# Kernel optimization log

Hardware: AMD Instinct MI355X
Metric: run time of the kernel (lower is better)

## Reference

```python
import jax, jax.numpy as jnp
import numpy as np
import math

N, E = 50000, 600000
IN_DIM, H, C, EDGE_DIM, OUT_DIM, PE_DIM = 128, 4, 32, 32, 64, 16
HC = H * C  # concat output dim of each TransformerConv layer


def _leaky(t):
    # nn.LeakyReLU default negative_slope = 0.01
    return jnp.where(t > 0, t, 0.01 * t)


def _conv(x, src, dst, edge_attr, Wq, bq, Wk, bk, Wv, bv, We, Wsk, bsk):
    """PyG TransformerConv (beta=False, concat=True, root_weight=True)."""
    n = x.shape[0]
    q = (x @ Wq + bq).reshape(n, H, C)
    k = (x @ Wk + bk).reshape(n, H, C)
    v = (x @ Wv + bv).reshape(n, H, C)
    e = (edge_attr @ We).reshape(-1, H, C)  # lin_edge has no bias
    k_j = k[src] + e                         # [E,H,C]
    alpha = jnp.einsum('ehc,ehc->eh', q[dst], k_j) / math.sqrt(C)  # [E,H]
    # segment softmax over incoming edges of each destination node
    m = jax.ops.segment_max(alpha, dst, num_segments=n)
    a = jnp.exp(alpha - m[dst])
    denom = jax.ops.segment_sum(a, dst, num_segments=n)
    a = a / denom[dst]
    v_j = v[src] + e                         # [E,H,C]
    out = jax.ops.segment_sum(a[..., None] * v_j, dst, num_segments=n)
    return out.reshape(n, HC) + x @ Wsk + bsk  # skip (root) connection


def setup_inputs() -> dict:
    key = jax.random.key(0)
    keys = iter(jax.random.split(key, 40))

    def nrm(shape, scale=1.0):
        return jax.random.normal(next(keys), shape, jnp.float32) * scale

    inp = {
        'x': nrm((N, IN_DIM)),
        'pe': nrm((N, PE_DIM)),
        'edge_index': jax.random.randint(next(keys), (2, E), 0, N),
        'edge_attr': nrm((E, EDGE_DIM)),
        'batch': jnp.zeros((N,), jnp.int32),
    }
    fins = [IN_DIM, HC]
    for l in range(2):
        fin = fins[l]
        s = 1.0 / math.sqrt(fin)
        se = 1.0 / math.sqrt(EDGE_DIM)
        for nm in ['Wq', 'Wk', 'Wv', 'Wsk']:
            inp[f'{nm}{l}'] = nrm((fin, HC), s)
        inp[f'We{l}'] = nrm((EDGE_DIM, HC), se)
        for nm in ['bq', 'bk', 'bv', 'bsk']:
            inp[f'{nm}{l}'] = jnp.zeros((HC,), jnp.float32)
    inp['W1'] = nrm((HC, C), 1.0 / math.sqrt(HC))
    inp['b1'] = jnp.zeros((C,), jnp.float32)
    inp['W2'] = nrm((C, OUT_DIM), 1.0 / math.sqrt(C))
    inp['b2'] = jnp.zeros((OUT_DIM,), jnp.float32)
    return inp


def reference(x, pe, edge_index, edge_attr, batch,
              Wq0, bq0, Wk0, bk0, Wv0, bv0, We0, Wsk0, bsk0,
              Wq1, bq1, Wk1, bk1, Wv1, bv1, We1, Wsk1, bsk1,
              W1, b1, W2, b2):
    src, dst = edge_index[0], edge_index[1]
    h = _leaky(_conv(x, src, dst, edge_attr, Wq0, bq0, Wk0, bk0, Wv0, bv0, We0, Wsk0, bsk0))
    h = _leaky(_conv(h, src, dst, edge_attr, Wq1, bq1, Wk1, bk1, Wv1, bv1, We1, Wsk1, bsk1))
    return _leaky(h @ W1 + b1) @ W2 + b2
```

## Files before the change

### kernel.cpp

```cpp
#include <hip/hip_runtime.h>
#include <hip/hip_bf16.h>
#include <math.h>

#define NN 50000
#define NE 600000

__global__ __launch_bounds__(256) void hist_kernel(const int* __restrict__ dst,
                                                   int* __restrict__ deg, int E) {
    int e = blockIdx.x * 256 + threadIdx.x;
    if (e < E) atomicAdd(&deg[dst[e]], 1);
}

__global__ __launch_bounds__(256) void scan_kernel(const int* __restrict__ deg,
                                                   int* __restrict__ indptr,
                                                   int* __restrict__ cursor, int n) {
    __shared__ int wsum[4];
    __shared__ int carry_s;
    const int tid = threadIdx.x, lane = tid & 63, wv = tid >> 6;
    if (tid == 0) carry_s = 0;
    __syncthreads();
    const int nceil = (n + 1023) & ~1023;
    for (int base = 0; base < nceil; base += 1024) {
        int i = base + tid * 4;
        int4 v = make_int4(0, 0, 0, 0);
        if (i + 3 < n) v = *(const int4*)(deg + i);
        else {
            if (i < n)     v.x = deg[i];
            if (i + 1 < n) v.y = deg[i + 1];
            if (i + 2 < n) v.z = deg[i + 2];
            if (i + 3 < n) v.w = deg[i + 3];
        }
        int tsum = v.x + v.y + v.z + v.w;
        int incl = tsum;
        #pragma unroll
        for (int off = 1; off < 64; off <<= 1) {
            int u = __shfl_up(incl, off);
            if (lane >= off) incl += u;
        }
        if (lane == 63) wsum[wv] = incl;
        __syncthreads();
        int wpre = 0;
        for (int w = 0; w < wv; ++w) wpre += wsum[w];
        int carry = carry_s;
        int start = carry + wpre + incl - tsum;
        if (i < n)     { indptr[i] = start;           cursor[i] = start; }
        int s1 = start + v.x;
        if (i + 1 < n) { indptr[i + 1] = s1;          cursor[i + 1] = s1; }
        int s2 = s1 + v.y;
        if (i + 2 < n) { indptr[i + 2] = s2;          cursor[i + 2] = s2; }
        int s3 = s2 + v.z;
        if (i + 3 < n) { indptr[i + 3] = s3;          cursor[i + 3] = s3; }
        __syncthreads();
        if (tid == 255) carry_s = carry + wpre + incl;
        __syncthreads();
    }
    if (tid == 0) indptr[n] = carry_s;
}

__global__ __launch_bounds__(256) void scatter_kernel(const int* __restrict__ src,
                                                      const int* __restrict__ dst,
                                                      int* __restrict__ cursor,
                                                      int* __restrict__ src_csr,
                                                      int* __restrict__ eid_csr, int E) {
    int e = blockIdx.x * 256 + threadIdx.x;
    if (e < E) {
        int d = dst[e];
        int slot = atomicAdd(&cursor[d], 1);
        src_csr[slot] = src[e];
        eid_csr[slot] = e;
    }
}

__global__ __launch_bounds__(256) void permute_ea(const int* __restrict__ eid_csr,
                                                  const float* __restrict__ ea,
                                                  float* __restrict__ ea_csr, int E) {
    int g = blockIdx.x * 256 + threadIdx.x;
    if (g < E * 8) {
        int slot = g >> 3, q = g & 7;
        int eid = eid_csr[slot];
        ((float4*)ea_csr)[(size_t)slot * 8 + q] = ((const float4*)ea)[(size_t)eid * 8 + q];
    }
}

__global__ __launch_bounds__(256, 4) void qkvsk_gemm(const float* __restrict__ X,
        const float* __restrict__ Wq,  const float* __restrict__ bq,
        const float* __restrict__ Wk,  const float* __restrict__ bk,
        const float* __restrict__ Wv,  const float* __restrict__ bv,
        const float* __restrict__ Wsk, const float* __restrict__ bsk,
        float* __restrict__ out, int nrows) {
    __shared__ float XsT[32][68];
    __shared__ float Ws[32][132];
    const int mat = blockIdx.y;
    const float* __restrict__ W;
    const float* __restrict__ bias;
    switch (mat) {
        case 0:  W = Wq;  bias = bq;  break;
        case 1:  W = Wk;  bias = bk;  break;
        case 2:  W = Wv;  bias = bv;  break;
        default: W = Wsk; bias = bsk; break;
    }
    const int n0 = blockIdx.x * 64;
    const int tid = threadIdx.x;
    const int tc = tid & 15;
    const int tr = tid >> 4;
    float acc[4][8];
    #pragma unroll
    for (int i = 0; i < 4; ++i)
        #pragma unroll
        for (int j = 0; j < 8; ++j) acc[i][j] = 0.f;

    #pragma unroll 1
    for (int k0 = 0; k0 < 128; k0 += 32) {
        #pragma unroll
        for (int c = 0; c < 2; ++c) {
            int lin4 = tid + c * 256;
            int row = lin4 >> 3, kq = lin4 & 7;
            int gr = n0 + row;
            float4 v = make_float4(0.f, 0.f, 0.f, 0.f);
            if (gr < nrows) v = ((const float4*)X)[(size_t)gr * 32 + (k0 >> 2) + kq];
            XsT[kq * 4 + 0][row] = v.x;
            XsT[kq * 4 + 1][row] = v.y;
            XsT[kq * 4 + 2][row] = v.z;
            XsT[kq * 4 + 3][row] = v.w;
        }
        #pragma unroll
        for (int c = 0; c < 4; ++c) {
            int lin4 = tid + c * 256;
            int row = lin4 >> 5, c4 = lin4 & 31;
            float4 v = ((const float4*)W)[(size_t)(k0 + row) * 32 + c4];
            Ws[row][c4 * 4 + 0] = v.x; Ws[row][c4 * 4 + 1] = v.y;
            Ws[row][c4 * 4 + 2] = v.z; Ws[row][c4 * 4 + 3] = v.w;
        }
        __syncthreads();
        #pragma unroll 8
        for (int k = 0; k < 32; ++k) {
            float4 xv = *(const float4*)&XsT[k][tr * 4];
            float4 w0 = *(const float4*)&Ws[k][tc * 8];
            float4 w1 = *(const float4*)&Ws[k][tc * 8 + 4];
            float xf[4] = {xv.x, xv.y, xv.z, xv.w};
            #pragma unroll
            for (int i = 0; i < 4; ++i) {
                acc[i][0] += xf[i] * w0.x; acc[i][1] += xf[i] * w0.y;
                acc[i][2] += xf[i] * w0.z; acc[i][3] += xf[i] * w0.w;
                acc[i][4] += xf[i] * w1.x; acc[i][5] += xf[i] * w1.y;
                acc[i][6] += xf[i] * w1.z; acc[i][7] += xf[i] * w1.w;
            }
        }
        __syncthreads();
    }
    float bfrag[8];
    #pragma unroll
    for (int j = 0; j < 8; ++j) bfrag[j] = bias[tc * 8 + j];
    #pragma unroll
    for (int i = 0; i < 4; ++i) {
        int gr = n0 + tr * 4 + i;
        if (gr < nrows) {
            float* orow = out + (size_t)gr * 512 + mat * 128 + tc * 8;
            float4 o0 = make_float4(acc[i][0] + bfrag[0], acc[i][1] + bfrag[1],
                                    acc[i][2] + bfrag[2], acc[i][3] + bfrag[3]);
            float4 o1 = make_float4(acc[i][4] + bfrag[4], acc[i][5] + bfrag[5],
                                    acc[i][6] + bfrag[6], acc[i][7] + bfrag[7]);
            *(float4*)orow = o0;
            *(float4*)(orow + 4) = o1;
        }
    }
}

template <bool PERM>
__global__ __launch_bounds__(256) void attn_kernel(const float* __restrict__ qkvsk,
                                                   const int* __restrict__ indptr,
                                                   const int* __restrict__ src_csr,
                                                   const int* __restrict__ eid_csr,
                                                   const float* __restrict__ ea,
                                                   const float* __restrict__ We,
                                                   float* __restrict__ hout, int nnodes) {
    __shared__ float We_s[32 * 128];
    for (int i = threadIdx.x; i < 1024; i += 256)
        ((float4*)We_s)[i] = ((const float4*)We)[i];
    __syncthreads();

    const int lane = threadIdx.x & 63;
    const int n = blockIdx.x * 4 + (threadIdx.x >> 6);
    if (n >= nnodes) return;

    const int d0 = lane * 2;
    const int h = lane >> 4;
    const int i0 = (lane & 15) * 2;

    const float2* nrow = (const float2*)(qkvsk + (size_t)n * 512);
    const float2 q2 = nrow[lane];

    float t0 = 0.f, t1 = 0.f;
    {
        const float4* qh = (const float4*)(qkvsk + (size_t)n * 512 + h * 32);
        #pragma unroll
        for (int c4 = 0; c4 < 8; ++c4) {
            float4 qv = qh[c4];
            int cb = h * 32 + c4 * 4;
            float4 w0 = *(const float4*)&We_s[i0 * 128 + cb];
            float4 w1 = *(const float4*)&We_s[(i0 + 1) * 128 + cb];
            t0 += qv.x * w0.x + qv.y * w0.y + qv.z * w0.z + qv.w * w0.w;
            t1 += qv.x * w1.x + qv.y * w1.y + qv.z * w1.z + qv.w * w1.w;
        }
    }

    float m = -INFINITY, ssum = 0.f;
    float accvx = 0.f, accvy = 0.f, accex = 0.f, accey = 0.f;
    const int s_end = indptr[n + 1];
    for (int s = indptr[n]; s < s_end; ++s) {
        int src = src_csr[s];
        size_t erow = PERM ? (size_t)s * 32 : (size_t)eid_csr[s] * 32;
        float2 ea2 = *(const float2*)(ea + erow + i0);
        const float2* srow = (const float2*)(qkvsk + (size_t)src * 512);
        float2 k2 = srow[64 + lane];
        float p = q2.x * k2.x + q2.y * k2.y + ea2.x * t0 + ea2.y * t1;
        p += __shfl_xor(p, 1);
        p += __shfl_xor(p, 2);
        p += __shfl_xor(p, 4);
        p += __shfl_xor(p, 8);
        float alpha = p * 0.17677669529663687f;
        float mnew = fmaxf(m, alpha);
        float sc = __expf(m - mnew);
        float a = __expf(alpha - mnew);
        m = mnew;
        ssum = ssum * sc + a;
        float2 v2 = srow[128 + lane];
        accvx = accvx * sc + a * v2.x;
        accvy = accvy * sc + a * v2.y;
        accex = accex * sc + a * ea2.x;
        accey = accey * sc + a * ea2.y;
    }

    float e0 = 0.f, e1 = 0.f;
    const int gbase = lane & 48;
    #pragma unroll
    for (int ii = 0; ii < 16; ++ii) {
        float ax = __shfl(accex, gbase + ii);
        float ay = __shfl(accey, gbase + ii);
        int ia = ii * 2;
        float2 wA = *(const float2*)&We_s[ia * 128 + d0];
        float2 wB = *(const float2*)&We_s[(ia + 1) * 128 + d0];
        e0 += ax * wA.x + ay * wB.x;
        e1 += ax * wA.y + ay * wB.y;
    }

    float inv = (ssum > 0.f) ? 1.0f / ssum : 0.f;
    float2 sk2 = nrow[192 + lane];
    float o0 = (accvx + e0) * inv + sk2.x;
    float o1 = (accvy + e1) * inv + sk2.y;
    o0 = o0 > 0.f ? o0 : 0.01f * o0;
    o1 = o1 > 0.f ? o1 : 0.01f * o1;
    ((float2*)(hout + (size_t)n * 128))[lane] = make_float2(o0, o1);
}

__global__ __launch_bounds__(256) void mlp_kernel(const float* __restrict__ h,
                                                  const float* __restrict__ W1,
                                                  const float* __restrict__ b1,
                                                  const float* __restrict__ W2,
                                                  const float* __restrict__ b2,
                                                  float* __restrict__ out, int nnodes) {
    __shared__ float W1s[128 * 32];
    __shared__ float W2s[32 * 64];
    __shared__ float b1s[32], b2s[64];
    for (int i = threadIdx.x; i < 1024; i += 256)
        ((float4*)W1s)[i] = ((const float4*)W1)[i];
    for (int i = threadIdx.x; i < 512; i += 256)
        ((float4*)W2s)[i] = ((const float4*)W2)[i];
    if (threadIdx.x < 32) b1s[threadIdx.x] = b1[threadIdx.x];
    if (threadIdx.x < 64) b2s[threadIdx.x] = b2[threadIdx.x];
    __syncthreads();

    const int j = threadIdx.x & 31;
    const int n = blockIdx.x * 8 + (threadIdx.x >> 5);
    if (n >= nnodes) return;

    const float4* h4 = (const float4*)(h + (size_t)n * 128);
    float t = b1s[j];
    #pragma unroll
    for (int k4 = 0; k4 < 32; ++k4) {
        float4 hv = h4[k4];
        t += hv.x * W1s[(k4 * 4 + 0) * 32 + j];
        t += hv.y * W1s[(k4 * 4 + 1) * 32 + j];
        t += hv.z * W1s[(k4 * 4 + 2) * 32 + j];
        t += hv.w * W1s[(k4 * 4 + 3) * 32 + j];
    }
    t = t > 0.f ? t : 0.01f * t;

    float o0 = b2s[j], o1 = b2s[j + 32];
    const int base = threadIdx.x & 32;
    #pragma unroll
    for (int c = 0; c < 32; ++c) {
        float tc = __shfl(t, base + c);
        o0 += tc * W2s[c * 64 + j];
        o1 += tc * W2s[c * 64 + j + 32];
    }
    out[(size_t)n * 64 + j] = o0;
    out[(size_t)n * 64 + j + 32] = o1;
}

extern "C" void kernel_launch(void* const* d_in, const int* in_sizes, int n_in,
                              void* d_out, int out_size, void* d_ws, size_t ws_size,
                              hipStream_t stream) {
    const float* x         = (const float*)d_in[0];
    const int*   edge_index= (const int*)d_in[2];
    const float* edge_attr = (const float*)d_in[3];
    const float* Wq0 = (const float*)d_in[5],  *Wk0 = (const float*)d_in[6];
    const float* Wv0 = (const float*)d_in[7],  *Wsk0= (const float*)d_in[8];
    const float* We0 = (const float*)d_in[9];
    const float* bq0 = (const float*)d_in[10], *bk0 = (const float*)d_in[11];
    const float* bv0 = (const float*)d_in[12], *bsk0= (const float*)d_in[13];
    const float* Wq1 = (const float*)d_in[14], *Wk1 = (const float*)d_in[15];
    const float* Wv1 = (const float*)d_in[16], *Wsk1= (const float*)d_in[17];
    const float* We1 = (const float*)d_in[18];
    const float* bq1 = (const float*)d_in[19], *bk1 = (const float*)d_in[20];
    const float* bv1 = (const float*)d_in[21], *bsk1= (const float*)d_in[22];
    const float* W1  = (const float*)d_in[23], *b1  = (const float*)d_in[24];
    const float* W2  = (const float*)d_in[25], *b2  = (const float*)d_in[26];

    const int N = in_sizes[0] / 128;
    const int E = in_sizes[2] / 2;
    const int* src = edge_index;
    const int* dst = edge_index + E;

    char* p = (char*)d_ws;
    size_t used = 0;
    auto alloc = [&](size_t bytes) {
        void* r = p + used;
        used += (bytes + 255) & ~(size_t)255;
        return r;
    };
    int*   indptr  = (int*)alloc((size_t)(N + 1) * 4);
    int*   deg     = (int*)alloc((size_t)N * 4);
    int*   cursor  = (int*)alloc((size_t)N * 4);
    int*   src_csr = (int*)alloc((size_t)E * 4);
    int*   eid_csr = (int*)alloc((size_t)E * 4);
    float* qkvsk   = (float*)alloc((size_t)N * 512 * 4);
    float* h0      = (float*)alloc((size_t)N * 128 * 4);
    float* h1      = (float*)alloc((size_t)N * 128 * 4);
    float* ea_csr  = (float*)alloc((size_t)E * 32 * 4);
    const bool perm_ok = (used <= ws_size);

    (void)hipMemsetAsync(deg, 0, (size_t)N * 4, stream);
    hist_kernel<<<(E + 255) / 256, 256, 0, stream>>>(dst, deg, E);
    scan_kernel<<<1, 256, 0, stream>>>(deg, indptr, cursor, N);
    scatter_kernel<<<(E + 255) / 256, 256, 0, stream>>>(src, dst, cursor, src_csr, eid_csr, E);
    if (perm_ok)
        permute_ea<<<((size_t)E * 8 + 255) / 256, 256, 0, stream>>>(eid_csr, edge_attr, ea_csr, E);

    dim3 ggrid((N + 63) / 64, 4);
    dim3 agrid((N + 3) / 4);

    qkvsk_gemm<<<ggrid, 256, 0, stream>>>(x, Wq0, bq0, Wk0, bk0, Wv0, bv0, Wsk0, bsk0, qkvsk, N);
    if (perm_ok)
        attn_kernel<true><<<agrid, 256, 0, stream>>>(qkvsk, indptr, src_csr, eid_csr, ea_csr, We0, h0, N);
    else
        attn_kernel<false><<<agrid, 256, 0, stream>>>(qkvsk, indptr, src_csr, eid_csr, edge_attr, We0, h0, N);

    qkvsk_gemm<<<ggrid, 256, 0, stream>>>(h0, Wq1, bq1, Wk1, bk1, Wv1, bv1, Wsk1, bsk1, qkvsk, N);
    if (perm_ok)
        attn_kernel<true><<<agrid, 256, 0, stream>>>(qkvsk, indptr, src_csr, eid_csr, ea_csr, We1, h1, N);
    else
        attn_kernel<false><<<agrid, 256, 0, stream>>>(qkvsk, indptr, src_csr, eid_csr, edge_attr, We1, h1, N);

    mlp_kernel<<<(N + 7) / 8, 256, 0, stream>>>(h1, W1, b1, W2, b2, (float*)d_out, N);
}
```

Measured before the change: 951.7 us.

## Split Q/skip and K/V buffers and process two edges per attention iteration

The projection output is split into two contiguous arrays, one holding Q and skip and one holding K and V. Each gathered source row in the attention loop then touches a single compact 1 KB span instead of two regions of a 2 KB row. The attention loop handles two edges per iteration with independent online-softmax states that are merged at the end, so more gathers are in flight at once. The shared-memory We tile is padded to a stride of 132 to reduce bank conflicts. The cost is extra registers for the second accumulator set, which may lower occupancy.

```diff
diff --git a/kernel.cpp b/kernel.cpp
--- a/kernel.cpp
+++ b/kernel.cpp
@@ -1,9 +1,6 @@
 #include <hip/hip_runtime.h>
 #include <hip/hip_bf16.h>
 #include <math.h>
-
-#define NN 50000
-#define NE 600000
 
 __global__ __launch_bounds__(256) void hist_kernel(const int* __restrict__ dst,
                                                    int* __restrict__ deg, int E) {
@@ -87,17 +84,19 @@
         const float* __restrict__ Wk,  const float* __restrict__ bk,
         const float* __restrict__ Wv,  const float* __restrict__ bv,
         const float* __restrict__ Wsk, const float* __restrict__ bsk,
-        float* __restrict__ out, int nrows) {
+        float* __restrict__ qsk, float* __restrict__ kv, int nrows) {
     __shared__ float XsT[32][68];
     __shared__ float Ws[32][132];
     const int mat = blockIdx.y;
     const float* __restrict__ W;
     const float* __restrict__ bias;
+    float* __restrict__ out;
+    int col;
     switch (mat) {
-        case 0:  W = Wq;  bias = bq;  break;
-        case 1:  W = Wk;  bias = bk;  break;
-        case 2:  W = Wv;  bias = bv;  break;
-        default: W = Wsk; bias = bsk; break;
+        case 0:  W = Wq;  bias = bq;  out = qsk; col = 0;   break;
+        case 1:  W = Wk;  bias = bk;  out = kv;  col = 0;   break;
+        case 2:  W = Wv;  bias = bv;  out = kv;  col = 128; break;
+        default: W = Wsk; bias = bsk; out = qsk; col = 128; break;
     }
     const int n0 = blockIdx.x * 64;
     const int tid = threadIdx.x;
@@ -155,7 +154,7 @@
     for (int i = 0; i < 4; ++i) {
         int gr = n0 + tr * 4 + i;
         if (gr < nrows) {
-            float* orow = out + (size_t)gr * 512 + mat * 128 + tc * 8;
+            float* orow = out + (size_t)gr * 256 + col + tc * 8;
             float4 o0 = make_float4(acc[i][0] + bfrag[0], acc[i][1] + bfrag[1],
                                     acc[i][2] + bfrag[2], acc[i][3] + bfrag[3]);
             float4 o1 = make_float4(acc[i][4] + bfrag[4], acc[i][5] + bfrag[5],
@@ -167,16 +166,20 @@
 }
 
 template <bool PERM>
-__global__ __launch_bounds__(256) void attn_kernel(const float* __restrict__ qkvsk,
+__global__ __launch_bounds__(256) void attn_kernel(const float* __restrict__ qsk,
+                                                   const float* __restrict__ kv,
                                                    const int* __restrict__ indptr,
                                                    const int* __restrict__ src_csr,
                                                    const int* __restrict__ eid_csr,
                                                    const float* __restrict__ ea,
                                                    const float* __restrict__ We,
                                                    float* __restrict__ hout, int nnodes) {
-    __shared__ float We_s[32 * 128];
-    for (int i = threadIdx.x; i < 1024; i += 256)
-        ((float4*)We_s)[i] = ((const float4*)We)[i];
+    __shared__ float We_s[32 * 132];
+    for (int i4 = threadIdx.x; i4 < 1024; i4 += 256) {
+        int r = i4 >> 5, c4 = i4 & 31;
+        float4 v = ((const float4*)We)[i4];
+        *((float4*)(We_s + r * 132 + c4 * 4)) = v;
+    }
     __syncthreads();
 
     const int lane = threadIdx.x & 63;
@@ -187,49 +190,106 @@
     const int h = lane >> 4;
     const int i0 = (lane & 15) * 2;
 
-    const float2* nrow = (const float2*)(qkvsk + (size_t)n * 512);
+    const float2* nrow = (const float2*)(qsk + (size_t)n * 256);
     const float2 q2 = nrow[lane];
 
     float t0 = 0.f, t1 = 0.f;
     {
-        const float4* qh = (const float4*)(qkvsk + (size_t)n * 512 + h * 32);
+        const float4* qh = (const float4*)(qsk + (size_t)n * 256 + h * 32);
         #pragma unroll
         for (int c4 = 0; c4 < 8; ++c4) {
             float4 qv = qh[c4];
             int cb = h * 32 + c4 * 4;
-            float4 w0 = *(const float4*)&We_s[i0 * 128 + cb];
-            float4 w1 = *(const float4*)&We_s[(i0 + 1) * 128 + cb];
+            float4 w0 = *(const float4*)&We_s[i0 * 132 + cb];
+            float4 w1 = *(const float4*)&We_s[(i0 + 1) * 132 + cb];
             t0 += qv.x * w0.x + qv.y * w0.y + qv.z * w0.z + qv.w * w0.w;
             t1 += qv.x * w1.x + qv.y * w1.y + qv.z * w1.z + qv.w * w1.w;
         }
     }
 
-    float m = -INFINITY, ssum = 0.f;
-    float accvx = 0.f, accvy = 0.f, accex = 0.f, accey = 0.f;
+    const float scale = 0.17677669529663687f;
+    float mA = -INFINITY, ssA = 0.f, avxA = 0.f, avyA = 0.f, aexA = 0.f, aeyA = 0.f;
+    float mB = -INFINITY, ssB = 0.f, avxB = 0.f, avyB = 0.f, aexB = 0.f, aeyB = 0.f;
+
+    int s = indptr[n];
     const int s_end = indptr[n + 1];
-    for (int s = indptr[n]; s < s_end; ++s) {
-        int src = src_csr[s];
-        size_t erow = PERM ? (size_t)s * 32 : (size_t)eid_csr[s] * 32;
-        float2 ea2 = *(const float2*)(ea + erow + i0);
-        const float2* srow = (const float2*)(qkvsk + (size_t)src * 512);
-        float2 k2 = srow[64 + lane];
-        float p = q2.x * k2.x + q2.y * k2.y + ea2.x * t0 + ea2.y * t1;
-        p += __shfl_xor(p, 1);
-        p += __shfl_xor(p, 2);
-        p += __shfl_xor(p, 4);
-        p += __shfl_xor(p, 8);
-        float alpha = p * 0.17677669529663687f;
-        float mnew = fmaxf(m, alpha);
-        float sc = __expf(m - mnew);
-        float a = __expf(alpha - mnew);
-        m = mnew;
-        ssum = ssum * sc + a;
-        float2 v2 = srow[128 + lane];
-        accvx = accvx * sc + a * v2.x;
-        accvy = accvy * sc + a * v2.y;
-        accex = accex * sc + a * ea2.x;
-        accey = accey * sc + a * ea2.y;
-    }
+    #pragma unroll 1
+    for (; s + 1 < s_end; s += 2) {
+        int srcA = src_csr[s];
+        int srcB = src_csr[s + 1];
+        size_t erowA = PERM ? (size_t)s * 32       : (size_t)eid_csr[s] * 32;
+        size_t erowB = PERM ? (size_t)(s + 1) * 32 : (size_t)eid_csr[s + 1] * 32;
+        float2 eaA = *(const float2*)(ea + erowA + i0);
+        float2 eaB = *(const float2*)(ea + erowB + i0);
+        const float2* rowA = (const float2*)(kv + (size_t)srcA * 256);
+        const float2* rowB = (const float2*)(kv + (size_t)srcB * 256);
+        float2 kA = rowA[lane];
+        float2 kB = rowB[lane];
+        float2 vA = rowA[64 + lane];
+        float2 vB = rowB[64 + lane];
+        float pA = q2.x * kA.x + q2.y * kA.y + eaA.x * t0 + eaA.y * t1;
+        float pB = q2.x * kB.x + q2.y * kB.y + eaB.x * t0 + eaB.y * t1;
+        pA += __shfl_xor(pA, 1);  pB += __shfl_xor(pB, 1);
+        pA += __shfl_xor(pA, 2);  pB += __shfl_xor(pB, 2);
+        pA += __shfl_xor(pA, 4);  pB += __shfl_xor(pB, 4);
+        pA += __shfl_xor(pA, 8);  pB += __shfl_xor(pB, 8);
+        float alA = pA * scale;
+        float alB = pB * scale;
+        {
+            float mn = fmaxf(mA, alA);
+            float sc = __expf(mA - mn);
+            float a  = __expf(alA - mn);
+            mA = mn;
+            ssA  = ssA  * sc + a;
+            avxA = avxA * sc + a * vA.x;
+            avyA = avyA * sc + a * vA.y;
+            aexA = aexA * sc + a * eaA.x;
+            aeyA = aeyA * sc + a * eaA.y;
+        }
+        {
+            float mn = fmaxf(mB, alB);
+            float sc = __expf(mB - mn);
+            float a  = __expf(alB - mn);
+            mB = mn;
+            ssB  = ssB  * sc + a;
+            avxB = avxB * sc + a * vB.x;
+            avyB = avyB * sc + a * vB.y;
+            aexB = aexB * sc + a * eaB.x;
+            aeyB = aeyB * sc + a * eaB.y;
+        }
+    }
+    if (s < s_end) {
+        int srcA = src_csr[s];
+        size_t erowA = PERM ? (size_t)s * 32 : (size_t)eid_csr[s] * 32;
+        float2 eaA = *(const float2*)(ea + erowA + i0);
+        const float2* rowA = (const float2*)(kv + (size_t)srcA * 256);
+        float2 kA = rowA[lane];
+        float2 vA = rowA[64 + lane];
+        float pA = q2.x * kA.x + q2.y * kA.y + eaA.x * t0 + eaA.y * t1;
+        pA += __shfl_xor(pA, 1);
+        pA += __shfl_xor(pA, 2);
+        pA += __shfl_xor(pA, 4);
+        pA += __shfl_xor(pA, 8);
+        float alA = pA * scale;
+        float mn = fmaxf(mA, alA);
+        float sc = __expf(mA - mn);
+        float a  = __expf(alA - mn);
+        mA = mn;
+        ssA  = ssA  * sc + a;
+        avxA = avxA * sc + a * vA.x;
+        avyA = avyA * sc + a * vA.y;
+        aexA = aexA * sc + a * eaA.x;
+        aeyA = aeyA * sc + a * eaA.y;
+    }
+
+    const float mm = fmaxf(mA, mB);
+    const float scA = (mA > -INFINITY) ? __expf(mA - mm) : 0.f;
+    const float scB = (mB > -INFINITY) ? __expf(mB - mm) : 0.f;
+    const float ssum  = ssA * scA + ssB * scB;
+    const float accvx = avxA * scA + avxB * scB;
+    const float accvy = avyA * scA + avyB * scB;
+    const float accex = aexA * scA + aexB * scB;
+    const float accey = aeyA * scA + aeyB * scB;
 
     float e0 = 0.f, e1 = 0.f;
     const int gbase = lane & 48;
@@ -238,14 +298,14 @@
         float ax = __shfl(accex, gbase + ii);
         float ay = __shfl(accey, gbase + ii);
         int ia = ii * 2;
-        float2 wA = *(const float2*)&We_s[ia * 128 + d0];
-        float2 wB = *(const float2*)&We_s[(ia + 1) * 128 + d0];
+        float2 wA = *(const float2*)&We_s[ia * 132 + d0];
+        float2 wB = *(const float2*)&We_s[(ia + 1) * 132 + d0];
         e0 += ax * wA.x + ay * wB.x;
         e1 += ax * wA.y + ay * wB.y;
     }
 
     float inv = (ssum > 0.f) ? 1.0f / ssum : 0.f;
-    float2 sk2 = nrow[192 + lane];
+    float2 sk2 = nrow[64 + lane];
     float o0 = (accvx + e0) * inv + sk2.x;
     float o1 = (accvy + e1) * inv + sk2.y;
     o0 = o0 > 0.f ? o0 : 0.01f * o0;
@@ -334,7 +394,8 @@
     int*   cursor  = (int*)alloc((size_t)N * 4);
     int*   src_csr = (int*)alloc((size_t)E * 4);
     int*   eid_csr = (int*)alloc((size_t)E * 4);
-    float* qkvsk   = (float*)alloc((size_t)N * 512 * 4);
+    float* qsk     = (float*)alloc((size_t)N * 256 * 4);
+    float* kvt     = (float*)alloc((size_t)N * 256 * 4);
     float* h0      = (float*)alloc((size_t)N * 128 * 4);
     float* h1      = (float*)alloc((size_t)N * 128 * 4);
     float* ea_csr  = (float*)alloc((size_t)E * 32 * 4);
@@ -350,17 +411,17 @@
     dim3 ggrid((N + 63) / 64, 4);
     dim3 agrid((N + 3) / 4);
 
-    qkvsk_gemm<<<ggrid, 256, 0, stream>>>(x, Wq0, bq0, Wk0, bk0, Wv0, bv0, Wsk0, bsk0, qkvsk, N);
+    qkvsk_gemm<<<ggrid, 256, 0, stream>>>(x, Wq0, bq0, Wk0, bk0, Wv0, bv0, Wsk0, bsk0, qsk, kvt, N);
     if (perm_ok)
-        attn_kernel<true><<<agrid, 256, 0, stream>>>(qkvsk, indptr, src_csr, eid_csr, ea_csr, We0, h0, N);
+        attn_kernel<true><<<agrid, 256, 0, stream>>>(qsk, kvt, indptr, src_csr, eid_csr, ea_csr, We0, h0, N);
     else
-        attn_kernel<false><<<agrid, 256, 0, stream>>>(qkvsk, indptr, src_csr, eid_csr, edge_attr, We0, h0, N);
-
-    qkvsk_gemm<<<ggrid, 256, 0, stream>>>(h0, Wq1, bq1, Wk1, bk1, Wv1, bv1, Wsk1, bsk1, qkvsk, N);
+        attn_kernel<false><<<agrid, 256, 0, stream>>>(qsk, kvt, indptr, src_csr, eid_csr, edge_attr, We0, h0, N);
+
+    qkvsk_gemm<<<ggrid, 256, 0, stream>>>(h0, Wq1, bq1, Wk1, bk1, Wv1, bv1, Wsk1, bsk1, qsk, kvt, N);
     if (perm_ok)
-        attn_kernel<true><<<agrid, 256, 0, stream>>>(qkvsk, indptr, src_csr, eid_csr, ea_csr, We1, h1, N);
+        attn_kernel<true><<<agrid, 256, 0, stream>>>(qsk, kvt, indptr, src_csr, eid_csr, ea_csr, We1, h1, N);
     else
-        attn_kernel<false><<<agrid, 256, 0, stream>>>(qkvsk, indptr, src_csr, eid_csr, edge_attr, We1, h1, N);
+        attn_kernel<false><<<agrid, 256, 0, stream>>>(qsk, kvt, indptr, src_csr, eid_csr, edge_attr, We1, h1, N);
 
     mlp_kernel<<<(N + 7) / 8, 256, 0, stream>>>(h1, W1, b1, W2, b2, (float*)d_out, N);
 }
```

New measurement: 817.8 us. -14.1%, faster.
